# Kernel optimization log

Hardware: AMD Instinct MI355X
Metric: run time of the kernel (lower is better)

## Reference

```python
import jax, jax.numpy as jnp
import numpy as np

D_MODEL = 1024
N_HEADS = 16
D_KEYS = 64
GROUP_POSITIONS = [list(range(g * 32, (g + 1) * 32)) for g in range(4)]


def _make_tables(group_positions, dim):
    # InGroup table: pe[j,i] = (j/Lg) * L0 / 10000^(2*(i//2)/dim)
    L0 = len(group_positions[0])
    rows = []
    for grp in group_positions:
        Lg = len(grp)
        for j in range(Lg):
            rows.append([j / Lg * L0 / np.power(10000.0, 2 * (i // 2) / dim) for i in range(dim)])
    pe = np.array(rows)
    ingroup = np.concatenate([np.sin(pe[:, 0::2]), np.cos(pe[:, 1::2])], axis=1).astype(np.float32)
    # Sequence (group) table: pe[j,i] = grp[0] / 10000^(j/Lg), constant over i
    rows = []
    for grp in group_positions:
        Lg = len(grp)
        for j in range(Lg):
            rows.append([grp[0] / np.power(10000.0, j / Lg) for _ in range(dim)])
    pe = np.array(rows)
    seq = np.concatenate([np.sin(pe[:, 0::2]), np.cos(pe[:, 1::2])], axis=1).astype(np.float32)
    return jnp.asarray(ingroup), jnp.asarray(seq)


def setup_inputs() -> dict:
    key = jax.random.key(0)
    ks = jax.random.split(key, 12)
    B, L, S = 64, 128, 128
    dqk = D_KEYS * N_HEADS
    sc_in = 1.0 / np.sqrt(D_MODEL)
    sc_out = 1.0 / np.sqrt(dqk)
    inp = {
        "queries": jax.random.normal(ks[0], (B, L, D_MODEL), jnp.float32),
        "keys": jax.random.normal(ks[1], (B, S, D_MODEL), jnp.float32),
        "values": jax.random.normal(ks[2], (B, S, D_MODEL), jnp.float32),
        "attn_mask": jnp.zeros((B, 1, L, S), dtype=bool),
        "Wq": jax.random.normal(ks[3], (D_MODEL, dqk), jnp.float32) * sc_in,
        "bq": jnp.zeros((dqk,), jnp.float32),
        "Wk": jax.random.normal(ks[4], (D_MODEL, dqk), jnp.float32) * sc_in,
        "bk": jnp.zeros((dqk,), jnp.float32),
        "Wv": jax.random.normal(ks[5], (D_MODEL, dqk), jnp.float32) * sc_in,
        "bv": jnp.zeros((dqk,), jnp.float32),
        "Wo": jax.random.normal(ks[6], (dqk, D_MODEL), jnp.float32) * sc_out,
        "bo": jnp.zeros((D_MODEL,), jnp.float32),
    }
    pos_ingroup, pos_seq = _make_tables(GROUP_POSITIONS, D_KEYS)
    inp["pos_ingroup"] = pos_ingroup  # [n_pos, d_keys]
    inp["pos_seq"] = pos_seq          # [n_pos, d_keys]
    return inp


def _rope(x, pos):
    # x: [B, H, L, D]; pos: [L, D]
    sin, cos = jnp.split(pos, 2, axis=-1)
    sin_pos = jnp.stack([sin, sin], axis=-1).reshape(pos.shape)
    cos_pos = jnp.stack([cos, cos], axis=-1).reshape(pos.shape)
    rot = jnp.stack([-x[..., 1::2], x[..., ::2]], axis=-1).reshape(x.shape)
    return x * cos_pos + rot * sin_pos


def reference(queries, keys, values, attn_mask, Wq, bq, Wk, bk, Wv, bv, Wo, bo, pos_ingroup, pos_seq):
    B, L, _ = queries.shape
    S = keys.shape[1]
    H, E = N_HEADS, D_KEYS
    q = (queries @ Wq + bq).reshape(B, L, H, E).transpose(0, 2, 1, 3)  # [B,H,L,E]
    k = (keys @ Wk + bk).reshape(B, S, H, E).transpose(0, 2, 1, 3)
    v = (values @ Wv + bv).reshape(B, S, H, E).transpose(0, 2, 1, 3)
    # group-sequence in-group RoPE, then group RoPE (tables gathered at arange positions)
    q = _rope(_rope(q, pos_ingroup[:L]), pos_seq[:L])
    k = _rope(_rope(k, pos_ingroup[:S]), pos_seq[:S])
    # inner full attention on [B,L,H,E] layout
    scale = 1.0 / jnp.sqrt(jnp.asarray(E, q.dtype))
    scores = jnp.einsum("bhle,bhse->bhls", q, k) * scale
    scores = jnp.where(attn_mask, jnp.asarray(-jnp.inf, scores.dtype), scores)
    attn = jax.nn.softmax(scores, axis=-1)  # [B,H,L,S]
    out = jnp.einsum("bhls,bhsd->blhd", attn, v).reshape(B, L, H * E)
    return out @ Wo + bo, attn
```

## Files before the change

### kernel.cpp

```cpp
#include <hip/hip_runtime.h>
#include <cstdint>

typedef float f32x4 __attribute__((ext_vector_type(4)));
typedef __bf16 bf16x8 __attribute__((ext_vector_type(8)));

typedef __attribute__((address_space(3))) uint32_t lds_u32;
typedef __attribute__((address_space(1))) const uint32_t glb_u32;

#define GLOAD_LDS16(gp, lp) \
  __builtin_amdgcn_global_load_lds((glb_u32*)(uintptr_t)(gp), (lds_u32*)(uintptr_t)(lp), 16, 0, 0)

__device__ inline unsigned short f2bf(float f) {
  union { float f; uint32_t u; } v; v.f = f;
  uint32_t u = v.u;
  return (unsigned short)((u + 0x7fffu + ((u >> 16) & 1u)) >> 16);
}

__global__ void prep_w(const float* __restrict__ wq, const float* __restrict__ wk,
                       const float* __restrict__ wv, const float* __restrict__ wo,
                       unsigned short* __restrict__ wt)
{
  __shared__ float t[64][65];
  const int z = blockIdx.z;
  const float* W = (z == 0) ? wq : (z == 1) ? wk : (z == 2) ? wv : wo;
  unsigned short* Wt = wt + (size_t)z * 1048576;
  const int n0 = blockIdx.x * 64, k0 = blockIdx.y * 64;
  const int tx = threadIdx.x & 63, ty = threadIdx.x >> 6;
#pragma unroll
  for (int i = 0; i < 16; i++) {
    int row = i * 4 + ty;
    t[row][tx] = W[(size_t)(k0 + row) * 1024 + n0 + tx];
  }
  __syncthreads();
#pragma unroll
  for (int i = 0; i < 16; i++) {
    int row = i * 4 + ty;
    Wt[(size_t)(n0 + row) * 1024 + k0 + tx] = f2bf(t[tx][row]);
  }
}

__global__ void comb_kernel(const float* __restrict__ ing, const float* __restrict__ seq,
                            float* __restrict__ cosc, float* __restrict__ sinc)
{
  int idx = blockIdx.x * 256 + threadIdx.x;
  int j = idx >> 5, i = idx & 31;
  float s1 = ing[j * 64 + i], c1 = ing[j * 64 + 32 + i];
  float s2 = seq[j * 64 + i], c2 = seq[j * 64 + 32 + i];
  cosc[idx] = c1 * c2 - s1 * s2;
  sinc[idx] = s1 * c2 + c1 * s2;
}

__global__ void cvt_kernel(const float* __restrict__ q, const float* __restrict__ k,
                           const float* __restrict__ v, unsigned short* __restrict__ dst)
{
  const int z = blockIdx.z;
  const float* src = (z == 0) ? q : (z == 1) ? k : v;
  unsigned short* d = dst + (size_t)z * 8388608;
  size_t i = ((size_t)blockIdx.x * 256 + threadIdx.x) * 4;
  float4 f = *(const float4*)&src[i];
  ushort4 o;
  o.x = f2bf(f.x); o.y = f2bf(f.y); o.z = f2bf(f.z); o.w = f2bf(f.w);
  *(ushort4*)&d[i] = o;
}

__global__ __launch_bounds__(256, 2)
void gemm_bt(const unsigned short* __restrict__ Abase,
             const unsigned short* __restrict__ Bbase,
             const float* __restrict__ b0, const float* __restrict__ b1,
             const float* __restrict__ b2,
             unsigned short* __restrict__ qb, unsigned short* __restrict__ kb,
             unsigned short* __restrict__ vtb,
             float* __restrict__ outf,
             const float* __restrict__ cosc, const float* __restrict__ sinc,
             int final_mode)
{
  __shared__ __attribute__((aligned(16))) unsigned short As[128 * 32];
  __shared__ __attribute__((aligned(16))) unsigned short Bs[128 * 32];

  const int tid = threadIdx.x;
  const int lane = tid & 63;
  const int wave = tid >> 6;
  const int quad = lane >> 4;
  const int l15 = lane & 15;

  const int z = blockIdx.z;
  const int tileN = blockIdx.x * 128;
  const int tileM = blockIdx.y * 128;
  const int K = 1024;

  const unsigned short* A = Abase + (size_t)z * (8192u * 1024u);
  const unsigned short* B = Bbase + (size_t)z * (1024u * 1024u);

  const int wm = (wave >> 1) * 64;
  const int wn = (wave & 1) * 64;

  f32x4 acc[4][4];
#pragma unroll
  for (int a = 0; a < 4; a++)
#pragma unroll
    for (int n = 0; n < 4; n++)
      acc[a][n] = (f32x4){0.f, 0.f, 0.f, 0.f};

  for (int k0 = 0; k0 < K; k0 += 32) {
#pragma unroll
    for (int cc0 = 0; cc0 < 2; cc0++) {
      int c = wave + cc0 * 4;
      int s = c * 64 + lane;
      int row = s >> 2;
      int koct = (s & 3) ^ ((row >> 1) & 3);
      const unsigned short* ga = A + (size_t)(tileM + row) * K + k0 + koct * 8;
      const unsigned short* gb = B + (size_t)(tileN + row) * K + k0 + koct * 8;
      GLOAD_LDS16(ga, &As[c * 512]);
      GLOAD_LDS16(gb, &Bs[c * 512]);
    }
    __syncthreads();

    bf16x8 af[4], bfr[4];
#pragma unroll
    for (int a = 0; a < 4; a++) {
      int r = wm + a * 16 + l15;
      int g = r * 4 + (quad ^ ((r >> 1) & 3));
      af[a] = *(const bf16x8*)&As[g * 8];
    }
#pragma unroll
    for (int n = 0; n < 4; n++) {
      int r = wn + n * 16 + l15;
      int g = r * 4 + (quad ^ ((r >> 1) & 3));
      bfr[n] = *(const bf16x8*)&Bs[g * 8];
    }
#pragma unroll
    for (int a = 0; a < 4; a++)
#pragma unroll
      for (int n = 0; n < 4; n++)
        acc[a][n] = __builtin_amdgcn_mfma_f32_16x16x32_bf16(af[a], bfr[n], acc[a][n], 0, 0, 0);
    __syncthreads();
  }

  if (final_mode) {
#pragma unroll
    for (int n = 0; n < 4; n++) {
      int cg = tileN + wn + n * 16 + l15;
      float bias = b0[cg];
#pragma unroll
      for (int a = 0; a < 4; a++)
#pragma unroll
        for (int reg = 0; reg < 4; reg++) {
          int r = tileM + wm + a * 16 + quad * 4 + reg;
          outf[(size_t)r * 1024 + cg] = acc[a][n][reg] + bias;
        }
    }
  } else {
    const float* bias = (z == 0) ? b0 : (z == 1) ? b1 : b2;
    unsigned short* outq = (z == 0) ? qb : kb;
#pragma unroll
    for (int n = 0; n < 4; n++) {
      int cg = tileN + wn + n * 16 + l15;
      float bv_ = bias[cg];
      int h = cg >> 6, e = cg & 63;
#pragma unroll
      for (int a = 0; a < 4; a++)
#pragma unroll
        for (int reg = 0; reg < 4; reg++) {
          int r = tileM + wm + a * 16 + quad * 4 + reg;
          int bb = r >> 7, l = r & 127;
          float v = acc[a][n][reg] + bv_;
          if (z == 2) {
            vtb[(((size_t)bb * 16 + h) * 64 + e) * 128 + l] = f2bf(v);
          } else {
            float other = __shfl_xor(v, 1);
            float cs = cosc[l * 32 + (e >> 1)];
            float sn = sinc[l * 32 + (e >> 1)];
            float res = v * cs + ((e & 1) ? other : -other) * sn;
            outq[(((size_t)bb * 16 + h) * 128 + l) * 64 + e] = f2bf(res);
          }
        }
    }
  }
}

__global__ __launch_bounds__(256, 2)
void attn_kernel(const unsigned short* __restrict__ qb,
                 const unsigned short* __restrict__ kb,
                 const unsigned short* __restrict__ vtb,
                 const unsigned char* __restrict__ mask,
                 float* __restrict__ attn_out,
                 unsigned short* __restrict__ ob)
{
  __shared__ __attribute__((aligned(16))) unsigned short Pb[128 * 136];
  const int tid = threadIdx.x;
  const int lane = tid & 63;
  const int wave = tid >> 6;
  const int quad = lane >> 4;
  const int l15 = lane & 15;
  const int bh = blockIdx.x;
  const int b = bh >> 4;
  const int h = bh & 15;

  const unsigned short* q = qb + (size_t)bh * 128 * 64;
  const unsigned short* k = kb + (size_t)bh * 128 * 64;
  const unsigned short* vt = vtb + (size_t)bh * 64 * 128;

  f32x4 sacc[2][8];
#pragma unroll
  for (int mt = 0; mt < 2; mt++)
#pragma unroll
    for (int nt = 0; nt < 8; nt++)
      sacc[mt][nt] = (f32x4){0.f, 0.f, 0.f, 0.f};

#pragma unroll
  for (int ks = 0; ks < 2; ks++) {
    bf16x8 aq[2], bk[8];
#pragma unroll
    for (int mt = 0; mt < 2; mt++)
      aq[mt] = *(const bf16x8*)&q[(size_t)(wave * 32 + mt * 16 + l15) * 64 + ks * 32 + quad * 8];
#pragma unroll
    for (int nt = 0; nt < 8; nt++)
      bk[nt] = *(const bf16x8*)&k[(size_t)(nt * 16 + l15) * 64 + ks * 32 + quad * 8];
#pragma unroll
    for (int mt = 0; mt < 2; mt++)
#pragma unroll
      for (int nt = 0; nt < 8; nt++)
        sacc[mt][nt] = __builtin_amdgcn_mfma_f32_16x16x32_bf16(aq[mt], bk[nt], sacc[mt][nt], 0, 0, 0);
  }

  const float scale = 0.125f;
#pragma unroll
  for (int mt = 0; mt < 2; mt++) {
#pragma unroll
    for (int reg = 0; reg < 4; reg++) {
      int r = wave * 32 + mt * 16 + quad * 4 + reg;
      const unsigned char* mrow = mask + ((size_t)b * 128 + r) * 128;
      float sv[8];
#pragma unroll
      for (int nt = 0; nt < 8; nt++) {
        float x = sacc[mt][nt][reg] * scale;
        if (mrow[nt * 16 + l15]) x = -__builtin_inff();
        sv[nt] = x;
      }
      float m = sv[0];
#pragma unroll
      for (int nt = 1; nt < 8; nt++) m = fmaxf(m, sv[nt]);
#pragma unroll
      for (int off = 1; off < 16; off <<= 1) m = fmaxf(m, __shfl_xor(m, off));
      float s = 0.f;
#pragma unroll
      for (int nt = 0; nt < 8; nt++) { sv[nt] = __expf(sv[nt] - m); s += sv[nt]; }
#pragma unroll
      for (int off = 1; off < 16; off <<= 1) s += __shfl_xor(s, off);
      float inv = 1.0f / s;
      float* arow = attn_out + ((size_t)bh * 128 + r) * 128;
#pragma unroll
      for (int nt = 0; nt < 8; nt++) {
        float p = sv[nt] * inv;
        arow[nt * 16 + l15] = p;
        Pb[r * 136 + nt * 16 + l15] = f2bf(p);
      }
    }
  }
  __syncthreads();

  f32x4 oacc[2][4];
#pragma unroll
  for (int mt = 0; mt < 2; mt++)
#pragma unroll
    for (int nt = 0; nt < 4; nt++)
      oacc[mt][nt] = (f32x4){0.f, 0.f, 0.f, 0.f};

#pragma unroll
  for (int ks = 0; ks < 4; ks++) {
    bf16x8 bv[4], ap[2];
#pragma unroll
    for (int nt = 0; nt < 4; nt++)
      bv[nt] = *(const bf16x8*)&vt[(size_t)(nt * 16 + l15) * 128 + ks * 32 + quad * 8];
#pragma unroll
    for (int mt = 0; mt < 2; mt++)
      ap[mt] = *(const bf16x8*)&Pb[(size_t)(wave * 32 + mt * 16 + l15) * 136 + ks * 32 + quad * 8];
#pragma unroll
    for (int mt = 0; mt < 2; mt++)
#pragma unroll
      for (int nt = 0; nt < 4; nt++)
        oacc[mt][nt] = __builtin_amdgcn_mfma_f32_16x16x32_bf16(ap[mt], bv[nt], oacc[mt][nt], 0, 0, 0);
  }

#pragma unroll
  for (int mt = 0; mt < 2; mt++)
#pragma unroll
    for (int nt = 0; nt < 4; nt++)
#pragma unroll
      for (int reg = 0; reg < 4; reg++) {
        int r = wave * 32 + mt * 16 + quad * 4 + reg;
        int e = nt * 16 + l15;
        ob[((size_t)b * 128 + r) * 1024 + h * 64 + e] = f2bf(oacc[mt][nt][reg]);
      }
}

extern "C" void kernel_launch(void* const* d_in, const int* in_sizes, int n_in,
                              void* d_out, int out_size, void* d_ws, size_t ws_size,
                              hipStream_t stream)
{
  const float* queries = (const float*)d_in[0];
  const float* keys    = (const float*)d_in[1];
  const float* values  = (const float*)d_in[2];
  const unsigned char* mask = (const unsigned char*)d_in[3];
  const float* Wq = (const float*)d_in[4];
  const float* bq = (const float*)d_in[5];
  const float* Wk = (const float*)d_in[6];
  const float* bk = (const float*)d_in[7];
  const float* Wv = (const float*)d_in[8];
  const float* bv = (const float*)d_in[9];
  const float* Wo = (const float*)d_in[10];
  const float* bo = (const float*)d_in[11];
  const float* ping = (const float*)d_in[12];
  const float* pseq = (const float*)d_in[13];

  float* out  = (float*)d_out;
  float* attn = out + 8388608;
  unsigned short* Xbf = (unsigned short*)attn;

  char* ws = (char*)d_ws;
  unsigned short* Wt  = (unsigned short*)(ws);
  float* cosc = (float*)(ws + 8388608);
  float* sinc = (float*)(ws + 8388608 + 16384);
  unsigned short* qbuf = (unsigned short*)(ws + 8421376);
  unsigned short* kbuf = (unsigned short*)(ws + 8421376 + 16777216);
  unsigned short* vtbuf= (unsigned short*)(ws + 8421376 + 2*16777216);
  unsigned short* obuf = (unsigned short*)(ws + 8421376 + 3*16777216);

  prep_w<<<dim3(16, 16, 4), 256, 0, stream>>>(Wq, Wk, Wv, Wo, Wt);
  comb_kernel<<<16, 256, 0, stream>>>(ping, pseq, cosc, sinc);
  cvt_kernel<<<dim3(8192, 1, 3), 256, 0, stream>>>(queries, keys, values, Xbf);
  gemm_bt<<<dim3(8, 64, 3), 256, 0, stream>>>(Xbf, Wt, bq, bk, bv,
                                              qbuf, kbuf, vtbuf, nullptr,
                                              cosc, sinc, 0);
  attn_kernel<<<dim3(1024), 256, 0, stream>>>(qbuf, kbuf, vtbuf, mask, attn, obuf);
  gemm_bt<<<dim3(8, 64, 1), 256, 0, stream>>>(obuf, Wt + 3 * 1048576, bo, bo, bo,
                                              qbuf, kbuf, vtbuf, out,
                                              cosc, sinc, 1);
}
```

Baseline: 381.6 us.

## Pre-swizzle GEMM operands into MFMA fragment layout and drop LDS staging

The conversion kernels (weights, inputs, and the attention output) now write bf16 data already arranged in per-wave MFMA fragment order. The GEMM can then load fragments straight from global memory with contiguous 16-byte loads, with no LDS staging and no barriers, and it runs at higher occupancy (launch bounds of 4). Removing the per-k-step syncs and LDS round trips is the goal. The cost is that operand reuse across waves now depends on L2/L1 caching rather than LDS. The final output store also becomes nontemporal.

```diff
diff --git a/kernel.cpp b/kernel.cpp
--- a/kernel.cpp
+++ b/kernel.cpp
@@ -3,12 +3,6 @@
 
 typedef float f32x4 __attribute__((ext_vector_type(4)));
 typedef __bf16 bf16x8 __attribute__((ext_vector_type(8)));
-
-typedef __attribute__((address_space(3))) uint32_t lds_u32;
-typedef __attribute__((address_space(1))) const uint32_t glb_u32;
-
-#define GLOAD_LDS16(gp, lp) \
-  __builtin_amdgcn_global_load_lds((glb_u32*)(uintptr_t)(gp), (lds_u32*)(uintptr_t)(lp), 16, 0, 0)
 
 __device__ inline unsigned short f2bf(float f) {
   union { float f; uint32_t u; } v; v.f = f;
@@ -16,27 +10,42 @@
   return (unsigned short)((u + 0x7fffu + ((u >> 16) & 1u)) >> 16);
 }
 
+
 __global__ void prep_w(const float* __restrict__ wq, const float* __restrict__ wk,
                        const float* __restrict__ wv, const float* __restrict__ wo,
                        unsigned short* __restrict__ wt)
 {
-  __shared__ float t[64][65];
+  __shared__ unsigned short Lt[128 * 72];
   const int z = blockIdx.z;
   const float* W = (z == 0) ? wq : (z == 1) ? wk : (z == 2) ? wv : wo;
   unsigned short* Wt = wt + (size_t)z * 1048576;
-  const int n0 = blockIdx.x * 64, k0 = blockIdx.y * 64;
-  const int tx = threadIdx.x & 63, ty = threadIdx.x >> 6;
-#pragma unroll
-  for (int i = 0; i < 16; i++) {
-    int row = i * 4 + ty;
-    t[row][tx] = W[(size_t)(k0 + row) * 1024 + n0 + tx];
+  const int nt = blockIdx.x;
+  const int k0 = blockIdx.y * 64;
+  const int n0 = nt * 128;
+  const int t = threadIdx.x;
+#pragma unroll
+  for (int p = 0; p < 8; p++) {
+    int kr = p * 8 + (t >> 5);
+    int nc = (t & 31) * 4;
+    float4 f = *(const float4*)&W[(size_t)(k0 + kr) * 1024 + n0 + nc];
+    Lt[(nc + 0) * 72 + kr] = f2bf(f.x);
+    Lt[(nc + 1) * 72 + kr] = f2bf(f.y);
+    Lt[(nc + 2) * 72 + kr] = f2bf(f.z);
+    Lt[(nc + 3) * 72 + kr] = f2bf(f.w);
   }
   __syncthreads();
 #pragma unroll
-  for (int i = 0; i < 16; i++) {
-    int row = i * 4 + ty;
-    Wt[(size_t)(n0 + row) * 1024 + k0 + tx] = f2bf(t[tx][row]);
-  }
+  for (int ktl = 0; ktl < 2; ktl++)
+#pragma unroll
+    for (int rep = 0; rep < 2; rep++) {
+      int pos = rep * 256 + t;
+      int half = pos >> 8, bn = (pos >> 6) & 3, lane = pos & 63;
+      int row = half * 64 + bn * 16 + (lane & 15);
+      int kc = ktl * 32 + (lane >> 4) * 8;
+      uint4 v = *(const uint4*)&Lt[row * 72 + kc];
+      *(uint4*)&Wt[(size_t)nt * 131072 + (blockIdx.y * 2 + ktl) * 4096 +
+                   half * 2048 + bn * 512 + lane * 8] = v;
+    }
 }
 
 __global__ void comb_kernel(const float* __restrict__ ing, const float* __restrict__ seq,
@@ -53,30 +62,46 @@
 __global__ void cvt_kernel(const float* __restrict__ q, const float* __restrict__ k,
                            const float* __restrict__ v, unsigned short* __restrict__ dst)
 {
+  __shared__ unsigned short Lt[128 * 136];
   const int z = blockIdx.z;
   const float* src = (z == 0) ? q : (z == 1) ? k : v;
-  unsigned short* d = dst + (size_t)z * 8388608;
-  size_t i = ((size_t)blockIdx.x * 256 + threadIdx.x) * 4;
-  float4 f = *(const float4*)&src[i];
-  ushort4 o;
-  o.x = f2bf(f.x); o.y = f2bf(f.y); o.z = f2bf(f.z); o.w = f2bf(f.w);
-  *(ushort4*)&d[i] = o;
-}
-
-__global__ __launch_bounds__(256, 2)
-void gemm_bt(const unsigned short* __restrict__ Abase,
-             const unsigned short* __restrict__ Bbase,
-             const float* __restrict__ b0, const float* __restrict__ b1,
-             const float* __restrict__ b2,
-             unsigned short* __restrict__ qb, unsigned short* __restrict__ kb,
-             unsigned short* __restrict__ vtb,
-             float* __restrict__ outf,
-             const float* __restrict__ cosc, const float* __restrict__ sinc,
-             int final_mode)
-{
-  __shared__ __attribute__((aligned(16))) unsigned short As[128 * 32];
-  __shared__ __attribute__((aligned(16))) unsigned short Bs[128 * 32];
-
+  unsigned short* d = dst + (size_t)z * 8388608 + (size_t)blockIdx.x * 131072;
+  const int kc = blockIdx.y;
+  const int t = threadIdx.x;
+#pragma unroll
+  for (int p = 0; p < 16; p++) {
+    int row = p * 8 + (t >> 5);
+    int col = (t & 31) * 4;
+    float4 f = *(const float4*)&src[((size_t)blockIdx.x * 128 + row) * 1024 + kc * 128 + col];
+    ushort4 u;
+    u.x = f2bf(f.x); u.y = f2bf(f.y); u.z = f2bf(f.z); u.w = f2bf(f.w);
+    *(ushort4*)&Lt[row * 136 + col] = u;
+  }
+  __syncthreads();
+#pragma unroll
+  for (int ktl = 0; ktl < 4; ktl++)
+#pragma unroll
+    for (int rep = 0; rep < 2; rep++) {
+      int pos = rep * 256 + t;
+      int half = pos >> 8, a = (pos >> 6) & 3, lane = pos & 63;
+      int row = half * 64 + a * 16 + (lane & 15);
+      int c = ktl * 32 + (lane >> 4) * 8;
+      uint4 vv = *(const uint4*)&Lt[row * 136 + c];
+      *(uint4*)&d[(size_t)(kc * 4 + ktl) * 4096 + half * 2048 + a * 512 + lane * 8] = vv;
+    }
+}
+
+__global__ __launch_bounds__(256, 4)
+void gemm_flat(const unsigned short* __restrict__ Abase,
+               const unsigned short* __restrict__ Bbase,
+               const float* __restrict__ b0, const float* __restrict__ b1,
+               const float* __restrict__ b2,
+               unsigned short* __restrict__ qb, unsigned short* __restrict__ kb,
+               unsigned short* __restrict__ vtb,
+               float* __restrict__ outf,
+               const float* __restrict__ cosc, const float* __restrict__ sinc,
+               int final_mode)
+{
   const int tid = threadIdx.x;
   const int lane = tid & 63;
   const int wave = tid >> 6;
@@ -84,15 +109,13 @@
   const int l15 = lane & 15;
 
   const int z = blockIdx.z;
-  const int tileN = blockIdx.x * 128;
-  const int tileM = blockIdx.y * 128;
-  const int K = 1024;
-
-  const unsigned short* A = Abase + (size_t)z * (8192u * 1024u);
-  const unsigned short* B = Bbase + (size_t)z * (1024u * 1024u);
-
-  const int wm = (wave >> 1) * 64;
-  const int wn = (wave & 1) * 64;
+  const int mt = blockIdx.x;
+  const int nt = blockIdx.y;
+
+  const unsigned short* A = Abase + (size_t)z * 8388608 + (size_t)mt * 131072 +
+                            (wave >> 1) * 2048 + lane * 8;
+  const unsigned short* B = Bbase + (size_t)z * 1048576 + (size_t)nt * 131072 +
+                            (wave & 1) * 2048 + lane * 8;
 
   f32x4 acc[4][4];
 #pragma unroll
@@ -101,41 +124,24 @@
     for (int n = 0; n < 4; n++)
       acc[a][n] = (f32x4){0.f, 0.f, 0.f, 0.f};
 
-  for (int k0 = 0; k0 < K; k0 += 32) {
-#pragma unroll
-    for (int cc0 = 0; cc0 < 2; cc0++) {
-      int c = wave + cc0 * 4;
-      int s = c * 64 + lane;
-      int row = s >> 2;
-      int koct = (s & 3) ^ ((row >> 1) & 3);
-      const unsigned short* ga = A + (size_t)(tileM + row) * K + k0 + koct * 8;
-      const unsigned short* gb = B + (size_t)(tileN + row) * K + k0 + koct * 8;
-      GLOAD_LDS16(ga, &As[c * 512]);
-      GLOAD_LDS16(gb, &Bs[c * 512]);
-    }
-    __syncthreads();
-
+#pragma unroll 4
+  for (int kt = 0; kt < 32; kt++) {
     bf16x8 af[4], bfr[4];
 #pragma unroll
-    for (int a = 0; a < 4; a++) {
-      int r = wm + a * 16 + l15;
-      int g = r * 4 + (quad ^ ((r >> 1) & 3));
-      af[a] = *(const bf16x8*)&As[g * 8];
-    }
-#pragma unroll
-    for (int n = 0; n < 4; n++) {
-      int r = wn + n * 16 + l15;
-      int g = r * 4 + (quad ^ ((r >> 1) & 3));
-      bfr[n] = *(const bf16x8*)&Bs[g * 8];
-    }
+    for (int a = 0; a < 4; a++)
+      af[a] = *(const bf16x8*)(A + kt * 4096 + a * 512);
+#pragma unroll
+    for (int n = 0; n < 4; n++)
+      bfr[n] = *(const bf16x8*)(B + kt * 4096 + n * 512);
 #pragma unroll
     for (int a = 0; a < 4; a++)
 #pragma unroll
       for (int n = 0; n < 4; n++)
         acc[a][n] = __builtin_amdgcn_mfma_f32_16x16x32_bf16(af[a], bfr[n], acc[a][n], 0, 0, 0);
-    __syncthreads();
-  }
-
+  }
+
+  const int tileM = mt * 128, tileN = nt * 128;
+  const int wm = (wave >> 1) * 64, wn = (wave & 1) * 64;
   if (final_mode) {
 #pragma unroll
     for (int n = 0; n < 4; n++) {
@@ -146,7 +152,7 @@
 #pragma unroll
         for (int reg = 0; reg < 4; reg++) {
           int r = tileM + wm + a * 16 + quad * 4 + reg;
-          outf[(size_t)r * 1024 + cg] = acc[a][n][reg] + bias;
+          __builtin_nontemporal_store(acc[a][n][reg] + bias, &outf[(size_t)r * 1024 + cg]);
         }
     }
   } else {
@@ -289,8 +295,10 @@
 #pragma unroll
       for (int reg = 0; reg < 4; reg++) {
         int r = wave * 32 + mt * 16 + quad * 4 + reg;
-        int e = nt * 16 + l15;
-        ob[((size_t)b * 128 + r) * 1024 + h * 64 + e] = f2bf(oacc[mt][nt][reg]);
+        int c = h * 64 + nt * 16 + l15;
+        size_t addr = (size_t)b * 131072 + (c >> 5) * 4096 + ((r >> 6) & 1) * 2048 +
+                      ((r >> 4) & 3) * 512 + ((((c >> 3) & 3) * 16) + (r & 15)) * 8 + (c & 7);
+        ob[addr] = f2bf(oacc[mt][nt][reg]);
       }
 }
 
@@ -315,7 +323,7 @@
 
   float* out  = (float*)d_out;
   float* attn = out + 8388608;
-  unsigned short* Xbf = (unsigned short*)attn;
+  unsigned short* Xs = (unsigned short*)attn;
 
   char* ws = (char*)d_ws;
   unsigned short* Wt  = (unsigned short*)(ws);
@@ -326,14 +334,14 @@
   unsigned short* vtbuf= (unsigned short*)(ws + 8421376 + 2*16777216);
   unsigned short* obuf = (unsigned short*)(ws + 8421376 + 3*16777216);
 
-  prep_w<<<dim3(16, 16, 4), 256, 0, stream>>>(Wq, Wk, Wv, Wo, Wt);
+  prep_w<<<dim3(8, 16, 4), 256, 0, stream>>>(Wq, Wk, Wv, Wo, Wt);
   comb_kernel<<<16, 256, 0, stream>>>(ping, pseq, cosc, sinc);
-  cvt_kernel<<<dim3(8192, 1, 3), 256, 0, stream>>>(queries, keys, values, Xbf);
-  gemm_bt<<<dim3(8, 64, 3), 256, 0, stream>>>(Xbf, Wt, bq, bk, bv,
-                                              qbuf, kbuf, vtbuf, nullptr,
-                                              cosc, sinc, 0);
+  cvt_kernel<<<dim3(64, 8, 3), 256, 0, stream>>>(queries, keys, values, Xs);
+  gemm_flat<<<dim3(64, 8, 3), 256, 0, stream>>>(Xs, Wt, bq, bk, bv,
+                                                qbuf, kbuf, vtbuf, nullptr,
+                                                cosc, sinc, 0);
   attn_kernel<<<dim3(1024), 256, 0, stream>>>(qbuf, kbuf, vtbuf, mask, attn, obuf);
-  gemm_bt<<<dim3(8, 64, 1), 256, 0, stream>>>(obuf, Wt + 3 * 1048576, bo, bo, bo,
-                                              qbuf, kbuf, vtbuf, out,
-                                              cosc, sinc, 1);
-}
+  gemm_flat<<<dim3(64, 8, 1), 256, 0, stream>>>(obuf, Wt + 3 * 1048576, bo, bo, bo,
+                                                qbuf, kbuf, vtbuf, out,
+                                                cosc, sinc, 1);
+}
```

Result: no change. 384.2 us (+0.7%).
